# Kernel tuning notes

Measured on AMD Instinct MI355X. Metric: run time of the kernel, lower is better.

## Reference

```python
import jax, jax.numpy as jnp
import numpy as np
from jax import lax

B, N, D = 32, 256, 128  # graphs, nodes-per-graph, embed_dim
T = B * N               # total nodes


def _mlp(x, W1, b1, W2, b2):
    # Linear -> ReLU -> Linear (query_proj / key_proj)
    return jnp.maximum(x @ W1.T + b1, 0.0) @ W2.T + b2


def _l2norm(x):
    # F.normalize(dim=-1), eps=1e-12
    return x / jnp.maximum(jnp.linalg.norm(x, axis=-1, keepdims=True), 1e-12)


def _gru_cell(x, h, W_ih, W_hh, b_ih, b_hh):
    # torch.nn.GRU single-step cell, gate order (r, z, n)
    gi = x @ W_ih.T + b_ih
    gh = h @ W_hh.T + b_hh
    ir, iz, inn = jnp.split(gi, 3, axis=-1)
    hr, hz, hn = jnp.split(gh, 3, axis=-1)
    r = jax.nn.sigmoid(ir + hr)
    z = jax.nn.sigmoid(iz + hz)
    n = jnp.tanh(inn + r * hn)
    return (1.0 - z) * n + z * h


def setup_inputs() -> dict:
    key = jax.random.key(0)
    ks = jax.random.split(key, 16)
    s = float(1.0 / np.sqrt(D))
    u = lambda k, sh: jax.random.uniform(k, sh, jnp.float32, -s, s)
    return {
        "node_embeddings": jax.random.normal(ks[0], (T, D), jnp.float32),
        "start_nodes": jnp.arange(B, dtype=jnp.int32) * N,  # first node of each graph
        "batch_idx": jnp.repeat(jnp.arange(B, dtype=jnp.int32), N),
        "Wq1": u(ks[1], (D, D)), "bq1": u(ks[2], (D,)),
        "Wq2": u(ks[3], (D, D)), "bq2": u(ks[4], (D,)),
        "Wk1": u(ks[5], (D, D)), "bk1": u(ks[6], (D,)),
        "Wk2": u(ks[7], (D, D)), "bk2": u(ks[8], (D,)),
        "W_ih": u(ks[9], (3 * D, D)), "W_hh": u(ks[10], (3 * D, D)),
        "b_ih": u(ks[11], (3 * D,)), "b_hh": u(ks[12], (3 * D,)),
        "v": jax.random.normal(ks[13], (D,), jnp.float32),
        "Wh": u(ks[14], (D, D)), "bh": u(ks[15], (D,)),
    }


def reference(node_embeddings, start_nodes, batch_idx, Wq1, bq1, Wq2, bq2,
              Wk1, bk1, Wk2, bk2, W_ih, W_hh, b_ih, b_hh, v, Wh, bh):
    Bn = start_nodes.shape[0]
    Tn = node_embeddings.shape[0]
    steps = Tn // Bn - 1  # equal-size graphs: N-1 decode steps after start node

    # graph contexts = per-graph mean of node embeddings -> hidden init
    ones = jnp.ones((Tn,), jnp.float32)
    counts = jax.ops.segment_sum(ones, batch_idx, num_segments=Bn)
    gctx = jax.ops.segment_sum(node_embeddings, batch_idx, num_segments=Bn) / counts[:, None]
    hidden0 = gctx @ Wh.T + bh                       # [B, D]

    # keys are recomputed identically every step in torch; hoist (same math)
    keys = _l2norm(_mlp(node_embeddings, Wk1, bk1, Wk2, bk2))  # [T, D]
    member = batch_idx[None, :] == jnp.arange(Bn)[:, None]     # [B, T]

    def step(carry, _):
        hidden, current, mask = carry
        mask = mask.at[current].set(False)           # visit current nodes
        x = node_embeddings[current]                 # [B, D]
        h = _gru_cell(x, hidden, W_ih, W_hh, b_ih, b_hh)
        q = _l2norm(_mlp(h, Wq1, bq1, Wq2, bq2))     # [B, D]
        # scores over ALL nodes, then masked to own-graph unvisited (as in torch)
        scores = jnp.einsum('btd,d->bt', jnp.tanh(keys[None] + q[:, None, :]), v)
        valid = member & mask[None, :]
        scores = jnp.where(valid, scores, -jnp.inf)
        probs = jax.nn.softmax(scores, axis=1)
        logp = jnp.log(probs + 1e-10)
        nxt = jnp.argmax(probs, axis=1).astype(current.dtype)  # eval-mode greedy
        lp = jnp.take_along_axis(logp, nxt[:, None], axis=1)[:, 0]
        return (h, nxt, mask), (current, lp)

    init = (hidden0, start_nodes, jnp.ones((Tn,), bool))
    (_, cur, _), (tour_steps, lps) = lax.scan(jax.checkpoint(step), init, None, length=steps)
    tours = jnp.concatenate([tour_steps, cur[None]], axis=0).T  # [B, N]
    log_probs = lps.T                                           # [B, N-1]
    return tours, log_probs
```

## Files before the change

kernel.cpp:

```cpp
#include <hip/hip_runtime.h>
#include <hip/hip_bf16.h>
#include <math.h>

#define DD   128
#define NPG  256
#define NGR  32
#define TTOT 8192
#define LOG2E  1.4426950408889634f
#define LOG2E2 2.8853900817779268f
#define KSTRIDE 264
#define SSTR    268
#define H2A(j)  ((j) + (((j)>>5)<<3))
#define PAD16(j) ((j) + (((j)>>4)<<2))

__device__ __forceinline__ float dot4(float4 a, float4 b){
  return a.x*b.x + a.y*b.y + a.z*b.z + a.w*b.w;
}
template<int CTRL, int RMASK>
__device__ __forceinline__ float upd_f(float oldv, float x){
  return __int_as_float(__builtin_amdgcn_update_dpp(
      __float_as_int(oldv), __float_as_int(x), CTRL, RMASK, 0xf, false));
}
__device__ __forceinline__ float dpp_xor1(float x){
  return __int_as_float(__builtin_amdgcn_mov_dpp(__float_as_int(x), 0xB1, 0xf, 0xf, false));
}
__device__ __forceinline__ float dpp_xor2(float x){
  return __int_as_float(__builtin_amdgcn_mov_dpp(__float_as_int(x), 0x4E, 0xf, 0xf, false));
}
__device__ __forceinline__ float quad_sum_dpp(float x){
  float s = x + dpp_xor1(x);
  return s + dpp_xor2(s);
}
__device__ __forceinline__ float dpp_wave_sum(float x){
  x += upd_f<0x111,0xf>(0.f, x);
  x += upd_f<0x112,0xf>(0.f, x);
  x += upd_f<0x114,0xf>(0.f, x);
  x += upd_f<0x118,0xf>(0.f, x);
  x += upd_f<0x142,0xa>(0.f, x);
  x += upd_f<0x143,0xc>(0.f, x);
  return __uint_as_float(__builtin_amdgcn_readlane(__float_as_uint(x), 63));
}
__device__ __forceinline__ float dpp_wave_max(float x){
  const float NI = -INFINITY;
  x = fmaxf(x, upd_f<0x111,0xf>(NI, x));
  x = fmaxf(x, upd_f<0x112,0xf>(NI, x));
  x = fmaxf(x, upd_f<0x114,0xf>(NI, x));
  x = fmaxf(x, upd_f<0x118,0xf>(NI, x));
  x = fmaxf(x, upd_f<0x142,0xa>(NI, x));
  x = fmaxf(x, upd_f<0x143,0xc>(NI, x));
  return __uint_as_float(__builtin_amdgcn_readlane(__float_as_uint(x), 63));
}
__device__ __forceinline__ float sigfast(float x){
  return __builtin_amdgcn_rcpf(1.f + __builtin_amdgcn_exp2f(-x*LOG2E));
}
__device__ __forceinline__ float tanhfast(float y){
  return 1.f - 2.f*__builtin_amdgcn_rcpf(1.f + __builtin_amdgcn_exp2f(y*LOG2E2));
}


__device__ __forceinline__ void load_w128(float* Ws, const float* __restrict__ W, int t){
  const float4* src = (const float4*)W;
  #pragma unroll
  for (int m=0;m<16;m++){
    int idx = m*256+t; int r = idx>>5, c4 = idx&31;
    float4 val = src[idx];
    float* dst = &Ws[r*129 + c4*4];
    dst[0]=val.x; dst[1]=val.y; dst[2]=val.z; dst[3]=val.w;
  }
}

__device__ __forceinline__ void mm_tile(const float* __restrict__ inS, const float* __restrict__ Ws,
                                        float acc[4][4], int jg, int ng){
  #pragma unroll
  for(int r=0;r<4;r++)
    #pragma unroll
    for(int c=0;c<4;c++) acc[r][c]=0.f;
  #pragma unroll 4
  for (int k=0;k<128;k++){
    float w[4], x[4];
    #pragma unroll
    for (int r=0;r<4;r++) w[r] = Ws[(jg*4+r)*129+k];
    #pragma unroll
    for (int c=0;c<4;c++) x[c] = inS[(ng*4+c)*129+k];
    #pragma unroll
    for (int r=0;r<4;r++)
      #pragma unroll
      for (int c=0;c<4;c++) acc[r][c] += w[r]*x[c];
  }
}

__global__ __launch_bounds__(256) void precompute_kernel(
    const float* __restrict__ emb,
    const float* __restrict__ Wk1, const float* __restrict__ bk1,
    const float* __restrict__ Wk2, const float* __restrict__ bk2,
    const float* __restrict__ Wih, const float* __restrict__ bih,
    float* __restrict__ keysE, float* __restrict__ giall)
{
  __shared__ __align__(16) float xs[32*129];
  __shared__ __align__(16) float Ws[128*129];
  __shared__ __align__(16) float hs[32*129];
  __shared__ __align__(16) float os[32*129];
  __shared__ float nrm[32];
  const int t  = threadIdx.x;
  const int n0 = blockIdx.x * 32;
  const int ng = t & 7, jg = t >> 3;

  {
    const float4* src = (const float4*)emb + (size_t)n0*32;
    #pragma unroll
    for (int m=0;m<4;m++){
      int idx = m*256+t; int n = idx>>5, c4 = idx&31;
      float4 val = src[idx];
      float* dst = &xs[n*129 + c4*4];
      dst[0]=val.x; dst[1]=val.y; dst[2]=val.z; dst[3]=val.w;
    }
  }
  load_w128(Ws, Wk1, t);
  __syncthreads();
  {
    float acc[4][4];
    mm_tile(xs, Ws, acc, jg, ng);
    #pragma unroll
    for (int r=0;r<4;r++){
      float bb = bk1[jg*4+r];
      #pragma unroll
      for (int c=0;c<4;c++) hs[(ng*4+c)*129 + jg*4+r] = fmaxf(acc[r][c]+bb, 0.f);
    }
  }
  __syncthreads();
  load_w128(Ws, Wk2, t);
  __syncthreads();
  {
    float acc[4][4];
    mm_tile(hs, Ws, acc, jg, ng);
    #pragma unroll
    for (int r=0;r<4;r++){
      float bb = bk2[jg*4+r];
      #pragma unroll
      for (int c=0;c<4;c++) os[(ng*4+c)*129 + jg*4+r] = acc[r][c]+bb;
    }
  }
  __syncthreads();
  if (t<32){
    float ss=0.f;
    for (int j=0;j<128;j++){ float x = os[t*129+j]; ss += x*x; }
    nrm[t] = fmaxf(sqrtf(ss), 1e-12f);
  }
  __syncthreads();
  #pragma unroll
  for (int m=0;m<16;m++){
    int idx = m*256+t; int nl = idx & 31, d = idx >> 5;
    float kk = os[nl*129 + d] / nrm[nl];
    keysE[(size_t)d*TTOT + n0 + nl] = __builtin_amdgcn_exp2f(kk * LOG2E2);
  }
  for (int c=0;c<3;c++){
    __syncthreads();
    load_w128(Ws, Wih + c*16384, t);
    __syncthreads();
    float acc[4][4];
    mm_tile(xs, Ws, acc, jg, ng);
    #pragma unroll
    for (int r=0;r<4;r++){
      float bb = bih[c*128 + jg*4+r];
      #pragma unroll
      for (int cc=0;cc<4;cc++)
        giall[(size_t)(n0 + ng*4+cc)*384 + c*128 + jg*4 + r] = acc[r][cc] + bb;
    }
  }
}


__global__ __launch_bounds__(512, 2) void decode_kernel(
    const float* __restrict__ emb,
    const float* __restrict__ keysE, const float* __restrict__ giall,
    const float* __restrict__ Whh, const float* __restrict__ bhh,
    const float* __restrict__ Wq1, const float* __restrict__ bq1,
    const float* __restrict__ Wq2, const float* __restrict__ bq2,
    const float* __restrict__ v,   const float* __restrict__ Wh,
    const float* __restrict__ bh,  const int* __restrict__ start_nodes,
    float* __restrict__ tours_o, float* __restrict__ lp_o)
{
  __shared__ __align__(16) float keys_s[128*KSTRIDE];
  __shared__ __align__(16) float h_s[2][160];
  __shared__ __align__(16) float qh_s[160];
  __shared__ __align__(16) float q_s[160];
  __shared__ __align__(16) float v_sp[160];
  __shared__ __align__(16) float spartS[8*SSTR];
  __shared__ int col2node_s[256], node2col_s[256];
  __shared__ float red2[8];

  const int t = threadIdx.x;
  const int b = blockIdx.x;
  const int g  = t >> 2, s3 = t & 3;
  const int w  = t >> 6, L  = t & 63;
  const int oct = L & 7, dgrp = L >> 3;

  float4 whh4[3][8], wq14[8], wq24[8];
  {
    const float4* w0  = (const float4*)(Whh + (size_t)(g      )*128 + s3*32);
    const float4* w1  = (const float4*)(Whh + (size_t)(128 + g)*128 + s3*32);
    const float4* w2  = (const float4*)(Whh + (size_t)(256 + g)*128 + s3*32);
    const float4* q1p = (const float4*)(Wq1 + (size_t)g*128 + s3*32);
    const float4* q2p = (const float4*)(Wq2 + (size_t)g*128 + s3*32);
    #pragma unroll
    for (int i=0;i<8;i++){
      whh4[0][i]=w0[i]; whh4[1][i]=w1[i]; whh4[2][i]=w2[i];
      wq14[i]=q1p[i];   wq24[i]=q2p[i];
    }
  }
  const float br = bhh[g], bz = bhh[128+g], bn = bhh[256+g];
  const float b1g = bq1[g], b2g = bq2[g];

  if (t<128) v_sp[PAD16(t)] = -2.f * v[t];
  if (t<256){ col2node_s[t] = t; node2col_s[t] = t; }
  {
    #pragma unroll
    for (int m=0;m<16;m++){
      int idx = m*512 + t; int d = idx>>6, q = idx&63;
      *(float4*)(keys_s + d*KSTRIDE + q*4) =
        *(const float4*)(keysE + (size_t)d*TTOT + b*256 + q*4);
    }
  }
  {
    int d = t & 127, part = t >> 7;
    float a = 0.f;
    const float* base = emb + (size_t)(b*256 + part*64)*128 + d;
    for (int i=0;i<64;i++) a += base[(size_t)i*128];
    spartS[part*128+d] = a;
  }
  int cur = start_nodes[b];
  __syncthreads();
  if (t<128){
    float a = 0.f;
    #pragma unroll
    for (int p=0;p<4;p++) a += spartS[p*128+t];
    q_s[t] = a * (1.f/256.f);
  }
  __syncthreads();
  if (t<128){
    float a = bh[t];
    const float* wr = Wh + (size_t)t*128;
    for (int k=0;k<128;k++) a += wr[k]*q_s[k];
    h_s[0][H2A(t)] = a;
  }
  {
    float xv = (t<128) ? v[t] : 0.f;
    float tot = dpp_wave_sum(xv);
    if (L==0) red2[w] = tot;
  }
  __syncthreads();
  float sv = 0.f;
  #pragma unroll
  for (int i=0;i<8;i++) sv += red2[i];

  float gir=0.f, giz=0.f, gin=0.f;
  if (s3==0){
    const float* gp = giall + (size_t)cur*384 + g;
    gir = gp[0]; giz = gp[128]; gin = gp[256];
  }

  for (int step=0; step<255; step++){
    const int par = step & 1;
    const int V   = 255 - step;
    const int curl = cur - b*256;

    if (t >= 128 && t < 256){
      int r = t - 128;
      int px = node2col_s[curl];
      keys_s[r*KSTRIDE + px] = keys_s[r*KSTRIDE + V];
    }
    if (t == 384) tours_o[b*256+step] = (float)cur;

    {
      float a0=0.f,a1=0.f,a2=0.f;
      const float4* hc4 = (const float4*)(h_s[par] + s3*40);
      #pragma unroll
      for (int i=0;i<8;i++){
        float4 hv = hc4[i];
        a0 += dot4(whh4[0][i], hv);
        a1 += dot4(whh4[1][i], hv);
        a2 += dot4(whh4[2][i], hv);
      }
      a0 = quad_sum_dpp(a0);
      a1 = quad_sum_dpp(a1);
      a2 = quad_sum_dpp(a2);
      if (s3==0){
        float r = sigfast(gir + a0 + br);
        float z = sigfast(giz + a1 + bz);
        float n = tanhfast(gin + r*(a2 + bn));
        h_s[par^1][H2A(g)] = (1.f-z)*n + z*h_s[par][H2A(g)];
      }
    }
    __syncthreads();

    if (t == 448){
      int px = node2col_s[curl];
      int ln = col2node_s[V];
      col2node_s[px] = ln;
      node2col_s[ln] = px;
    }

    {
      float a=0.f;
      const float4* hc4 = (const float4*)(h_s[par^1] + s3*40);
      #pragma unroll
      for (int i=0;i<8;i++) a += dot4(wq14[i], hc4[i]);
      a = quad_sum_dpp(a);
      if (s3==0) qh_s[H2A(g)] = fmaxf(a + b1g, 0.f);
    }
    __syncthreads();

    {
      float a=0.f;
      const float4* qc4 = (const float4*)(qh_s + s3*40);
      #pragma unroll
      for (int i=0;i<8;i++) a += dot4(wq24[i], qc4[i]);
      a = quad_sum_dpp(a);
      float qval = a + b2g;
      if (s3==0) q_s[PAD16(g)] = qval;
      float ssp = (s3==0) ? qval*qval : 0.f;
      float tot = dpp_wave_sum(ssp);
      if (L==0) red2[w] = tot;
    }
    __syncthreads();

    if (32*w < V){
      float ss = 0.f;
      #pragma unroll
      for (int i=0;i<8;i++) ss += red2[i];
      float rn = 1.f / fmaxf(sqrtf(ss), 1e-12f);
      const float* kbase = keys_s + dgrp*16*KSTRIDE + 32*w + oct*4;
      const float* qb    = q_s  + dgrp*20;
      const float* vbase = v_sp + dgrp*20;
      float4 acc = {0.f,0.f,0.f,0.f};
      #pragma unroll
      for (int jj=0;jj<16;jj++){
        float eqj = __builtin_amdgcn_exp2f(qb[jj] * rn * LOG2E2);
        float vj  = vbase[jj];
        float4 K = *(const float4*)(kbase + jj*KSTRIDE);
        float r0 = __builtin_amdgcn_rcpf(fmaf(K.x, eqj, 1.f));
        float r1 = __builtin_amdgcn_rcpf(fmaf(K.y, eqj, 1.f));
        float r2 = __builtin_amdgcn_rcpf(fmaf(K.z, eqj, 1.f));
        float r3 = __builtin_amdgcn_rcpf(fmaf(K.w, eqj, 1.f));
        acc.x = fmaf(vj, r0, acc.x);
        acc.y = fmaf(vj, r1, acc.y);
        acc.z = fmaf(vj, r2, acc.z);
        acc.w = fmaf(vj, r3, acc.w);
      }
      *(float4*)(spartS + dgrp*SSTR + 32*w + oct*4) = acc;
    }
    __syncthreads();

    {
      const float* sp = spartS + 4*L;
      float sx=0.f, sy=0.f, sz=0.f, sw=0.f;
      #pragma unroll
      for (int i=0;i<8;i++){
        float4 p = *(const float4*)(sp + i*SSTR);
        sx += p.x; sy += p.y; sz += p.z; sw += p.w;
      }
      int c0 = 4*L;
      float vx = (c0+0 < V) ? sv+sx : -INFINITY;
      float vy = (c0+1 < V) ? sv+sy : -INFINITY;
      float vz = (c0+2 < V) ? sv+sz : -INFINITY;
      float vw = (c0+3 < V) ? sv+sw : -INFINITY;
      float bm = vx; int bc = c0;
      if (vy > bm){ bm=vy; bc=c0+1; }
      if (vz > bm){ bm=vz; bc=c0+2; }
      if (vw > bm){ bm=vw; bc=c0+3; }
      float m = dpp_wave_max(bm);
      unsigned long long mk = __ballot(bm == m);
      int flane = __ffsll(mk) - 1;
      int besti = __builtin_amdgcn_readlane(bc, flane);
      float es = __builtin_amdgcn_exp2f((vx-m)*LOG2E) + __builtin_amdgcn_exp2f((vy-m)*LOG2E)
               + __builtin_amdgcn_exp2f((vz-m)*LOG2E) + __builtin_amdgcn_exp2f((vw-m)*LOG2E);
      float S = dpp_wave_sum(es);
      cur = b*256 + col2node_s[besti];
      if (s3==0){
        const float* gp = giall + (size_t)cur*384 + g;
        gir = gp[0]; giz = gp[128]; gin = gp[256];
      }
      if (t==320) lp_o[b*255+step] = logf(1.f/S + 1e-10f);
    }
  }
  if (t==0) tours_o[b*256+255] = (float)cur;

  (void)oct;
}

extern "C" void kernel_launch(void* const* d_in, const int* in_sizes, int n_in,
                              void* d_out, int out_size, void* d_ws, size_t ws_size,
                              hipStream_t stream) {
  const float* emb  = (const float*)d_in[0];
  const int*   startn = (const int*)d_in[1];
  const float* Wq1 = (const float*)d_in[3];  const float* bq1 = (const float*)d_in[4];
  const float* Wq2 = (const float*)d_in[5];  const float* bq2 = (const float*)d_in[6];
  const float* Wk1 = (const float*)d_in[7];  const float* bk1 = (const float*)d_in[8];
  const float* Wk2 = (const float*)d_in[9];  const float* bk2 = (const float*)d_in[10];
  const float* Wih = (const float*)d_in[11]; const float* Whh = (const float*)d_in[12];
  const float* bih = (const float*)d_in[13]; const float* bhh = (const float*)d_in[14];
  const float* v   = (const float*)d_in[15]; const float* Wh  = (const float*)d_in[16];
  const float* bh  = (const float*)d_in[17];

  float* keysE = (float*)d_ws;
  float* giall = keysE + (size_t)TTOT*DD;

  float* outp = (float*)d_out;

  precompute_kernel<<<256, 256, 0, stream>>>(emb, Wk1, bk1, Wk2, bk2, Wih, bih, keysE, giall);
  decode_kernel<<<NGR, 512, 0, stream>>>(emb, keysE, giall, Whh, bhh, Wq1, bq1, Wq2, bq2,
                                         v, Wh, bh, startn, outp, outp + TTOT);
}
```

Before: 886.4 us.

## Keep column/node permutation in registers, buffer outputs in LDS, prefetch gi rows

```diff
diff --git a/kernel.cpp b/kernel.cpp
--- a/kernel.cpp
+++ b/kernel.cpp
@@ -186,8 +186,9 @@
   __shared__ __align__(16) float q_s[160];
   __shared__ __align__(16) float v_sp[160];
   __shared__ __align__(16) float spartS[8*SSTR];
-  __shared__ int col2node_s[256], node2col_s[256];
   __shared__ float red2[8];
+  __shared__ float tour_s[256];
+  __shared__ float lp_s[256];
 
   const int t = threadIdx.x;
   const int b = blockIdx.x;
@@ -211,8 +212,10 @@
   const float br = bhh[g], bz = bhh[128+g], bn = bhh[256+g];
   const float b1g = bq1[g], b2g = bq2[g];
 
+  int c2n0 = 4*L, c2n1 = 4*L+1, c2n2 = 4*L+2, c2n3 = 4*L+3;
+  int n2c0 = 4*L, n2c1 = 4*L+1, n2c2 = 4*L+2, n2c3 = 4*L+3;
+
   if (t<128) v_sp[PAD16(t)] = -2.f * v[t];
-  if (t<256){ col2node_s[t] = t; node2col_s[t] = t; }
   {
     #pragma unroll
     for (int m=0;m<16;m++){
@@ -228,6 +231,16 @@
     for (int i=0;i<64;i++) a += base[(size_t)i*128];
     spartS[part*128+d] = a;
   }
+  {
+    const float4* gw = (const float4*)(giall + (size_t)b*256*384);
+    float wx=0.f, wy=0.f, wz=0.f, ww=0.f;
+    #pragma unroll 4
+    for (int i=t; i<24576; i+=512){
+      float4 xq = gw[i];
+      wx+=xq.x; wy+=xq.y; wz+=xq.z; ww+=xq.w;
+    }
+    asm volatile("" :: "v"(wx), "v"(wy), "v"(wz), "v"(ww));
+  }
   int cur = start_nodes[b];
   __syncthreads();
   if (t<128){
@@ -252,6 +265,8 @@
   float sv = 0.f;
   #pragma unroll
   for (int i=0;i<8;i++) sv += red2[i];
+  float hg = 0.f;
+  if (s3==0) hg = h_s[0][H2A(g)];
 
   float gir=0.f, giz=0.f, gin=0.f;
   if (s3==0){
@@ -264,12 +279,28 @@
     const int V   = 255 - step;
     const int curl = cur - b*256;
 
+    int selp = (curl&2) ? ((curl&1)?n2c3:n2c2) : ((curl&1)?n2c1:n2c0);
+    const int px = __builtin_amdgcn_readlane(selp, curl>>2);
+    int selc = (V&2) ? ((V&1)?c2n3:c2n2) : ((V&1)?c2n1:c2n0);
+    const int ln = __builtin_amdgcn_readlane(selc, V>>2);
+    {
+      const bool mp = (L == (px>>2)); const int pq = px & 3;
+      c2n0 = (mp && pq==0) ? ln : c2n0;
+      c2n1 = (mp && pq==1) ? ln : c2n1;
+      c2n2 = (mp && pq==2) ? ln : c2n2;
+      c2n3 = (mp && pq==3) ? ln : c2n3;
+      const bool ml = (L == (ln>>2)); const int lq = ln & 3;
+      n2c0 = (ml && lq==0) ? px : n2c0;
+      n2c1 = (ml && lq==1) ? px : n2c1;
+      n2c2 = (ml && lq==2) ? px : n2c2;
+      n2c3 = (ml && lq==3) ? px : n2c3;
+    }
+
     if (t >= 128 && t < 256){
       int r = t - 128;
-      int px = node2col_s[curl];
       keys_s[r*KSTRIDE + px] = keys_s[r*KSTRIDE + V];
     }
-    if (t == 384) tours_o[b*256+step] = (float)cur;
+    if (t == 384) tour_s[step] = (float)cur;
 
     {
       float a0=0.f,a1=0.f,a2=0.f;
@@ -288,17 +319,12 @@
         float r = sigfast(gir + a0 + br);
         float z = sigfast(giz + a1 + bz);
         float n = tanhfast(gin + r*(a2 + bn));
-        h_s[par^1][H2A(g)] = (1.f-z)*n + z*h_s[par][H2A(g)];
+        float hnew = (1.f-z)*n + z*hg;
+        h_s[par^1][H2A(g)] = hnew;
+        hg = hnew;
       }
     }
     __syncthreads();
-
-    if (t == 448){
-      int px = node2col_s[curl];
-      int ln = col2node_s[V];
-      col2node_s[px] = ln;
-      node2col_s[ln] = px;
-    }
 
     {
       float a=0.f;
@@ -324,42 +350,47 @@
     }
     __syncthreads();
 
-    if (32*w < V){
-      float ss = 0.f;
-      #pragma unroll
-      for (int i=0;i<8;i++) ss += red2[i];
-      float rn = 1.f / fmaxf(sqrtf(ss), 1e-12f);
-      const float* kbase = keys_s + dgrp*16*KSTRIDE + 32*w + oct*4;
-      const float* qb    = q_s  + dgrp*20;
-      const float* vbase = v_sp + dgrp*20;
-      float4 acc = {0.f,0.f,0.f,0.f};
-      #pragma unroll
-      for (int jj=0;jj<16;jj++){
-        float eqj = __builtin_amdgcn_exp2f(qb[jj] * rn * LOG2E2);
-        float vj  = vbase[jj];
-        float4 K = *(const float4*)(kbase + jj*KSTRIDE);
-        float r0 = __builtin_amdgcn_rcpf(fmaf(K.x, eqj, 1.f));
-        float r1 = __builtin_amdgcn_rcpf(fmaf(K.y, eqj, 1.f));
-        float r2 = __builtin_amdgcn_rcpf(fmaf(K.z, eqj, 1.f));
-        float r3 = __builtin_amdgcn_rcpf(fmaf(K.w, eqj, 1.f));
-        acc.x = fmaf(vj, r0, acc.x);
-        acc.y = fmaf(vj, r1, acc.y);
-        acc.z = fmaf(vj, r2, acc.z);
-        acc.w = fmaf(vj, r3, acc.w);
+    {
+      const int co = 32*w + oct*4;
+      if (co < V){
+        float ss = 0.f;
+        #pragma unroll
+        for (int i=0;i<8;i++) ss += red2[i];
+        float rn = 1.f / fmaxf(sqrtf(ss), 1e-12f);
+        const float* kbase = keys_s + dgrp*16*KSTRIDE + co;
+        const float* qb    = q_s  + dgrp*20;
+        const float* vbase = v_sp + dgrp*20;
+        float4 acc = {0.f,0.f,0.f,0.f};
+        #pragma unroll
+        for (int jj=0;jj<16;jj++){
+          float eqj = __builtin_amdgcn_exp2f(qb[jj] * rn * LOG2E2);
+          float vj  = vbase[jj];
+          float4 K = *(const float4*)(kbase + jj*KSTRIDE);
+          float r0 = __builtin_amdgcn_rcpf(fmaf(K.x, eqj, 1.f));
+          float r1 = __builtin_amdgcn_rcpf(fmaf(K.y, eqj, 1.f));
+          float r2 = __builtin_amdgcn_rcpf(fmaf(K.z, eqj, 1.f));
+          float r3 = __builtin_amdgcn_rcpf(fmaf(K.w, eqj, 1.f));
+          acc.x = fmaf(vj, r0, acc.x);
+          acc.y = fmaf(vj, r1, acc.y);
+          acc.z = fmaf(vj, r2, acc.z);
+          acc.w = fmaf(vj, r3, acc.w);
+        }
+        *(float4*)(spartS + dgrp*SSTR + co) = acc;
       }
-      *(float4*)(spartS + dgrp*SSTR + 32*w + oct*4) = acc;
-    }
-    __syncthreads();
-
-    {
-      const float* sp = spartS + 4*L;
+    }
+    __syncthreads();
+
+    {
+      const int c0 = 4*L;
       float sx=0.f, sy=0.f, sz=0.f, sw=0.f;
-      #pragma unroll
-      for (int i=0;i<8;i++){
-        float4 p = *(const float4*)(sp + i*SSTR);
-        sx += p.x; sy += p.y; sz += p.z; sw += p.w;
+      if (c0 < V){
+        const float* sp = spartS + c0;
+        #pragma unroll
+        for (int i=0;i<8;i++){
+          float4 p = *(const float4*)(sp + i*SSTR);
+          sx += p.x; sy += p.y; sz += p.z; sw += p.w;
+        }
       }
-      int c0 = 4*L;
       float vx = (c0+0 < V) ? sv+sx : -INFINITY;
       float vy = (c0+1 < V) ? sv+sy : -INFINITY;
       float vz = (c0+2 < V) ? sv+sz : -INFINITY;
@@ -372,20 +403,22 @@
       unsigned long long mk = __ballot(bm == m);
       int flane = __ffsll(mk) - 1;
       int besti = __builtin_amdgcn_readlane(bc, flane);
-      float es = __builtin_amdgcn_exp2f((vx-m)*LOG2E) + __builtin_amdgcn_exp2f((vy-m)*LOG2E)
-               + __builtin_amdgcn_exp2f((vz-m)*LOG2E) + __builtin_amdgcn_exp2f((vw-m)*LOG2E);
-      float S = dpp_wave_sum(es);
-      cur = b*256 + col2node_s[besti];
+      int seln = (besti&2) ? ((besti&1)?c2n3:c2n2) : ((besti&1)?c2n1:c2n0);
+      cur = b*256 + __builtin_amdgcn_readlane(seln, besti>>2);
       if (s3==0){
         const float* gp = giall + (size_t)cur*384 + g;
         gir = gp[0]; giz = gp[128]; gin = gp[256];
       }
-      if (t==320) lp_o[b*255+step] = logf(1.f/S + 1e-10f);
-    }
-  }
-  if (t==0) tours_o[b*256+255] = (float)cur;
-
-  (void)oct;
+      float es = __builtin_amdgcn_exp2f((vx-m)*LOG2E) + __builtin_amdgcn_exp2f((vy-m)*LOG2E)
+               + __builtin_amdgcn_exp2f((vz-m)*LOG2E) + __builtin_amdgcn_exp2f((vw-m)*LOG2E);
+      float S = dpp_wave_sum(es);
+      if (t==320) lp_s[step] = logf(1.f/S + 1e-10f);
+    }
+  }
+  if (t==0) tour_s[255] = (float)cur;
+  __syncthreads();
+  if (t < 256)      tours_o[b*256 + t] = tour_s[t];
+  else if (t < 511) lp_o[b*255 + (t-256)] = lp_s[t-256];
 }
 
 extern "C" void kernel_launch(void* const* d_in, const int* in_sizes, int n_in,
```

New measurement: 975.4 us. 1.1x slower.

## Add a helper wavefront for key swaps, tour writes and log-prob softmax

Applied to the files above, without the earlier changes.

```diff
diff --git a/kernel.cpp b/kernel.cpp
--- a/kernel.cpp
+++ b/kernel.cpp
@@ -170,7 +170,7 @@
 }
 
 
-__global__ __launch_bounds__(512, 2) void decode_kernel(
+__global__ __launch_bounds__(576, 2) void decode_kernel(
     const float* __restrict__ emb,
     const float* __restrict__ keysE, const float* __restrict__ giall,
     const float* __restrict__ Whh, const float* __restrict__ bhh,
@@ -194,26 +194,28 @@
   const int g  = t >> 2, s3 = t & 3;
   const int w  = t >> 6, L  = t & 63;
   const int oct = L & 7, dgrp = L >> 3;
+  const bool mainw = (t < 512);
+  const int gE = mainw ? g : 0;
 
   float4 whh4[3][8], wq14[8], wq24[8];
   {
-    const float4* w0  = (const float4*)(Whh + (size_t)(g      )*128 + s3*32);
-    const float4* w1  = (const float4*)(Whh + (size_t)(128 + g)*128 + s3*32);
-    const float4* w2  = (const float4*)(Whh + (size_t)(256 + g)*128 + s3*32);
-    const float4* q1p = (const float4*)(Wq1 + (size_t)g*128 + s3*32);
-    const float4* q2p = (const float4*)(Wq2 + (size_t)g*128 + s3*32);
+    const float4* w0  = (const float4*)(Whh + (size_t)(gE      )*128 + s3*32);
+    const float4* w1  = (const float4*)(Whh + (size_t)(128 + gE)*128 + s3*32);
+    const float4* w2  = (const float4*)(Whh + (size_t)(256 + gE)*128 + s3*32);
+    const float4* q1p = (const float4*)(Wq1 + (size_t)gE*128 + s3*32);
+    const float4* q2p = (const float4*)(Wq2 + (size_t)gE*128 + s3*32);
     #pragma unroll
     for (int i=0;i<8;i++){
       whh4[0][i]=w0[i]; whh4[1][i]=w1[i]; whh4[2][i]=w2[i];
       wq14[i]=q1p[i];   wq24[i]=q2p[i];
     }
   }
-  const float br = bhh[g], bz = bhh[128+g], bn = bhh[256+g];
-  const float b1g = bq1[g], b2g = bq2[g];
+  const float br = bhh[gE], bz = bhh[128+gE], bn = bhh[256+gE];
+  const float b1g = bq1[gE], b2g = bq2[gE];
 
   if (t<128) v_sp[PAD16(t)] = -2.f * v[t];
   if (t<256){ col2node_s[t] = t; node2col_s[t] = t; }
-  {
+  if (mainw){
     #pragma unroll
     for (int m=0;m<16;m++){
       int idx = m*512 + t; int d = idx>>6, q = idx&63;
@@ -221,7 +223,7 @@
         *(const float4*)(keysE + (size_t)d*TTOT + b*256 + q*4);
     }
   }
-  {
+  if (mainw){
     int d = t & 127, part = t >> 7;
     float a = 0.f;
     const float* base = emb + (size_t)(b*256 + part*64)*128 + d;
@@ -246,7 +248,7 @@
   {
     float xv = (t<128) ? v[t] : 0.f;
     float tot = dpp_wave_sum(xv);
-    if (L==0) red2[w] = tot;
+    if (L==0 && w<8) red2[w] = tot;
   }
   __syncthreads();
   float sv = 0.f;
@@ -254,7 +256,7 @@
   for (int i=0;i<8;i++) sv += red2[i];
 
   float gir=0.f, giz=0.f, gin=0.f;
-  if (s3==0){
+  if (s3==0 && mainw){
     const float* gp = giall + (size_t)cur*384 + g;
     gir = gp[0]; giz = gp[128]; gin = gp[256];
   }
@@ -264,14 +266,14 @@
     const int V   = 255 - step;
     const int curl = cur - b*256;
 
-    if (t >= 128 && t < 256){
-      int r = t - 128;
+    if (w == 8){
+      if (L == 0) tours_o[b*256+step] = (float)cur;
       int px = node2col_s[curl];
-      keys_s[r*KSTRIDE + px] = keys_s[r*KSTRIDE + V];
-    }
-    if (t == 384) tours_o[b*256+step] = (float)cur;
-
-    {
+      keys_s[L*KSTRIDE + px]       = keys_s[L*KSTRIDE + V];
+      keys_s[(L+64)*KSTRIDE + px]  = keys_s[(L+64)*KSTRIDE + V];
+    }
+
+    if (mainw){
       float a0=0.f,a1=0.f,a2=0.f;
       const float4* hc4 = (const float4*)(h_s[par] + s3*40);
       #pragma unroll
@@ -293,14 +295,14 @@
     }
     __syncthreads();
 
-    if (t == 448){
+    if (t == 512){
       int px = node2col_s[curl];
       int ln = col2node_s[V];
       col2node_s[px] = ln;
       node2col_s[ln] = px;
     }
 
-    {
+    if (mainw){
       float a=0.f;
       const float4* hc4 = (const float4*)(h_s[par^1] + s3*40);
       #pragma unroll
@@ -310,7 +312,7 @@
     }
     __syncthreads();
 
-    {
+    if (mainw){
       float a=0.f;
       const float4* qc4 = (const float4*)(qh_s + s3*40);
       #pragma unroll
@@ -372,15 +374,17 @@
       unsigned long long mk = __ballot(bm == m);
       int flane = __ffsll(mk) - 1;
       int besti = __builtin_amdgcn_readlane(bc, flane);
-      float es = __builtin_amdgcn_exp2f((vx-m)*LOG2E) + __builtin_amdgcn_exp2f((vy-m)*LOG2E)
-               + __builtin_amdgcn_exp2f((vz-m)*LOG2E) + __builtin_amdgcn_exp2f((vw-m)*LOG2E);
-      float S = dpp_wave_sum(es);
       cur = b*256 + col2node_s[besti];
-      if (s3==0){
+      if (s3==0 && mainw){
         const float* gp = giall + (size_t)cur*384 + g;
         gir = gp[0]; giz = gp[128]; gin = gp[256];
       }
-      if (t==320) lp_o[b*255+step] = logf(1.f/S + 1e-10f);
+      if (w == 8){
+        float es = __builtin_amdgcn_exp2f((vx-m)*LOG2E) + __builtin_amdgcn_exp2f((vy-m)*LOG2E)
+                 + __builtin_amdgcn_exp2f((vz-m)*LOG2E) + __builtin_amdgcn_exp2f((vw-m)*LOG2E);
+        float S = dpp_wave_sum(es);
+        if (L == 1) lp_o[b*255+step] = logf(1.f/S + 1e-10f);
+      }
     }
   }
   if (t==0) tours_o[b*256+255] = (float)cur;
@@ -408,6 +412,6 @@
   float* outp = (float*)d_out;
 
   precompute_kernel<<<256, 256, 0, stream>>>(emb, Wk1, bk1, Wk2, bk2, Wih, bih, keysE, giall);
-  decode_kernel<<<NGR, 512, 0, stream>>>(emb, keysE, giall, Whh, bhh, Wq1, bq1, Wq2, bq2,
+  decode_kernel<<<NGR, 576, 0, stream>>>(emb, keysE, giall, Whh, bhh, Wq1, bq1, Wq2, bq2,
                                          v, Wh, bh, startn, outp, outp + TTOT);
 }
```

After: 2.284 ms. 2.58x slower.
